# Performance work log

Measured on AMD Instinct MI355X. Metric: run time of the kernel, lower is better.

The kernel has to match this reference:

```python
import jax, jax.numpy as jnp
import numpy as np

B, L, EMBED = 8, 4096, 1024
HEADS, WIN, SHIFT = 16, 128, 64
HD = EMBED // HEADS
MLP_HIDDEN = 4 * EMBED
SCALE = HD ** -0.5
NW = L // WIN


def _layer_norm(x, w, b, eps=1e-5):
    m = x.mean(-1, keepdims=True)
    v = x.var(-1, keepdims=True)
    return (x - m) * jax.lax.rsqrt(v + eps) * w + b


def _compute_mask():
    # replicate SwinBlock1D._compute_mask: region ids over full L, then windowed
    sizes = [L - WIN, WIN - SHIFT, SHIFT]
    region = np.zeros(L, np.int32)
    pos = 0
    for i, s in enumerate(sizes):
        region[pos:pos + s] = i
        pos += s
    region = region.reshape(NW, WIN)
    diff = region[:, None, :] - region[:, :, None]  # (nW, W, W)
    return jnp.asarray(np.where(diff != 0, -100.0, 0.0).astype(np.float32))


_MASK = _compute_mask()
_REL_IDX = jnp.arange(WIN)[None, :] - jnp.arange(WIN)[:, None] + WIN - 1  # (W, W)


def setup_inputs() -> dict:
    key = jax.random.key(0)
    ks = jax.random.split(key, 8)
    s = 0.02

    def w(k, shape):
        return jax.random.normal(k, shape, jnp.float32) * s

    return {
        "x": jax.random.normal(ks[0], (B, L, EMBED), jnp.float32),
        "qkv_w": w(ks[1], (3 * EMBED, EMBED)),
        "qkv_b": jnp.zeros((3 * EMBED,), jnp.float32),
        "proj_w": w(ks[2], (EMBED, EMBED)),
        "proj_b": jnp.zeros((EMBED,), jnp.float32),
        "rpb": w(ks[3], (2 * WIN - 1, HEADS)),
        "norm1_w": jnp.ones((EMBED,), jnp.float32),
        "norm1_b": jnp.zeros((EMBED,), jnp.float32),
        "norm2_w": jnp.ones((EMBED,), jnp.float32),
        "norm2_b": jnp.zeros((EMBED,), jnp.float32),
        "mlp_w1": w(ks[4], (MLP_HIDDEN, EMBED)),
        "mlp_b1": jnp.zeros((MLP_HIDDEN,), jnp.float32),
        "mlp_w2": w(ks[5], (EMBED, MLP_HIDDEN)),
        "mlp_b2": jnp.zeros((EMBED,), jnp.float32),
    }


def reference(x, qkv_w, qkv_b, proj_w, proj_b, rpb,
              norm1_w, norm1_b, norm2_w, norm2_b,
              mlp_w1, mlp_b1, mlp_w2, mlp_b2):
    BW = B * NW
    shortcut = x
    h = _layer_norm(x, norm1_w, norm1_b)
    # shifted-window attention (shift_size > 0)
    h = jnp.roll(h, -SHIFT, axis=1)
    win = h.reshape(BW, WIN, EMBED)
    qkv = (win @ qkv_w.T + qkv_b).reshape(BW, WIN, 3, HEADS, HD)
    qkv = qkv.transpose(2, 0, 3, 1, 4)  # (3, BW, H, W, hd)
    q, k, v = qkv[0], qkv[1], qkv[2]
    attn = jnp.einsum('bhqd,bhkd->bhqk', q, k) * SCALE
    bias = rpb[_REL_IDX]  # (W, W, H)
    attn = attn + bias.transpose(2, 0, 1)[None]
    attn = attn.reshape(B, NW, HEADS, WIN, WIN) + _MASK[None, :, None]
    attn = jax.nn.softmax(attn.reshape(BW, HEADS, WIN, WIN), axis=-1)
    # dropout layers are identity in eval mode
    out = jnp.einsum('bhqk,bhkd->bhqd', attn, v)
    out = out.transpose(0, 2, 1, 3).reshape(BW, WIN, EMBED)
    out = out @ proj_w.T + proj_b
    out = out.reshape(B, L, EMBED)
    out = jnp.roll(out, SHIFT, axis=1)
    x = shortcut + out
    # MLP block
    h2 = _layer_norm(x, norm2_w, norm2_b)
    h2 = jax.nn.gelu(h2 @ mlp_w1.T + mlp_b1, approximate=False) @ mlp_w2.T + mlp_b2
    return x + h2
```

## Files before the change

### kernel.cpp

```cpp
#include <hip/hip_runtime.h>
#include <cstdint>
#include <cstddef>

#define SEQ_L   4096
#define EMBED   1024
#define HEADS   16
#define WINSZ   128
#define SHIFTSZ 64
#define HD      64
#define NWIN    32
#define MTOT    32768
#define ATT_SCALE 0.125f

typedef __bf16 bf16x8 __attribute__((ext_vector_type(8)));
typedef float  f32x4  __attribute__((ext_vector_type(4)));

typedef __attribute__((address_space(3))) void       lds_void;
typedef const __attribute__((address_space(1))) void gbl_void;

#define GLDS16(g, s) __builtin_amdgcn_global_load_lds((gbl_void*)(g), (lds_void*)(s), 16, 0, 0)

__device__ __forceinline__ unsigned short f2bf(float f) {
    unsigned int u = __float_as_uint(f);
    u += 0x7fffu + ((u >> 16) & 1u);
    return (unsigned short)(u >> 16);
}

__launch_bounds__(256)
__global__ void wconv(const float* __restrict__ in, unsigned short* __restrict__ out, int n)
{
    const int i = (blockIdx.x * 256 + threadIdx.x) * 4;
    if (i < n) {
        const float4 v = *(const float4*)(in + i);
        ushort4 o;
        o.x = f2bf(v.x); o.y = f2bf(v.y); o.z = f2bf(v.z); o.w = f2bf(v.w);
        *(ushort4*)(out + i) = o;
    }
}

__launch_bounds__(256)
__global__ void ln_kernel(const float* __restrict__ x, const float* __restrict__ gw,
                          const float* __restrict__ gb, unsigned short* __restrict__ out,
                          int shift)
{
    const int row  = blockIdx.x * 4 + (threadIdx.x >> 6);
    const int lane = threadIdx.x & 63;
    const int b    = row >> 12;
    const int lw   = row & 4095;
    const int src  = (b << 12) | ((lw + shift) & 4095);
    const float* xr = x + (size_t)src * EMBED;

    float4 v[4];
    float s = 0.f, q = 0.f;
#pragma unroll
    for (int j = 0; j < 4; ++j) {
        v[j] = ((const float4*)xr)[lane + j * 64];
        s += v[j].x + v[j].y + v[j].z + v[j].w;
        q += v[j].x * v[j].x + v[j].y * v[j].y + v[j].z * v[j].z + v[j].w * v[j].w;
    }
#pragma unroll
    for (int off = 32; off > 0; off >>= 1) {
        s += __shfl_xor(s, off);
        q += __shfl_xor(q, off);
    }
    const float mean = s * (1.0f / 1024.0f);
    const float rstd = rsqrtf(q * (1.0f / 1024.0f) - mean * mean + 1e-5f);

    unsigned short* orow = out + (size_t)row * EMBED;
#pragma unroll
    for (int j = 0; j < 4; ++j) {
        const float4 w4 = ((const float4*)gw)[lane + j * 64];
        const float4 b4 = ((const float4*)gb)[lane + j * 64];
        ushort4 o;
        o.x = f2bf((v[j].x - mean) * rstd * w4.x + b4.x);
        o.y = f2bf((v[j].y - mean) * rstd * w4.y + b4.y);
        o.z = f2bf((v[j].z - mean) * rstd * w4.z + b4.z);
        o.w = f2bf((v[j].w - mean) * rstd * w4.w + b4.w);
        ((ushort4*)orow)[lane + j * 64] = o;
    }
}


__device__ __forceinline__ void stage_half(const unsigned short* __restrict__ g, int ldk,
                                           char* ldsbase, int tid)
{
    const int r  = tid >> 3;
    const int cg = ((tid & 7) ^ (r & 7)) << 3;
    GLDS16(g + (size_t)r        * ldk + cg, ldsbase + tid * 16);
    GLDS16(g + (size_t)(r + 64) * ldk + cg, ldsbase + 8192 + tid * 16);
}

__device__ __forceinline__ bf16x8 lds_frag(const char* half, int row, int koff)
{
    const int off = koff ^ ((row & 7) << 4);
    return *(const bf16x8*)(half + row * 128 + off);
}

template<int EPI>
__launch_bounds__(512, 2)
__global__ void gemm256(const unsigned short* __restrict__ A, const unsigned short* __restrict__ W,
                        const float* __restrict__ bias, void* __restrict__ outv,
                        const float* __restrict__ resid, int M, int N, int K)
{
    __shared__ __align__(16) char lds[131072];
    const int tid = threadIdx.x;
    const int l   = tid & 63, w = tid >> 6;
    const int wm  = w >> 2, wn = w & 3;
    const int lr  = l & 15, hi = l >> 4;
    const int k0off = hi << 4;
    const int br0   = (wn & 1) << 6;

    int id = blockIdx.x;
    const int nwg = gridDim.x;
    id = (id & 7) * (nwg >> 3) + (id >> 3);
    const int Ntl = N >> 8;
    const int m0  = (id / Ntl) << 8;
    const int n0  = (id % Ntl) << 8;
    const int NT  = K >> 6;

#define HTB(b, ab, h) (lds + ((((b) << 1 | (ab)) << 1 | (h)) << 14))

    stage_half(A + (size_t)m0         * K,      K, HTB(0,0,0), tid);
    stage_half(A + (size_t)(m0 + 128) * K,      K, HTB(0,0,1), tid);
    stage_half(W + (size_t)n0         * K,      K, HTB(0,1,0), tid);
    stage_half(W + (size_t)(n0 + 128) * K,      K, HTB(0,1,1), tid);
    stage_half(W + (size_t)n0         * K + 64, K, HTB(1,1,0), tid);
    stage_half(W + (size_t)(n0 + 128) * K + 64, K, HTB(1,1,1), tid);
    asm volatile("s_waitcnt vmcnt(4)" ::: "memory");
    __builtin_amdgcn_s_barrier();

    f32x4 acc[8][4];
#pragma unroll
    for (int f = 0; f < 8; ++f)
#pragma unroll
        for (int n = 0; n < 4; ++n)
            acc[f][n] = (f32x4){0.f, 0.f, 0.f, 0.f};

    bf16x8 bf[4][2], af0[2][2], af1[2][2];

#define LOAD_A_BANK(bank, AHP, F0)                                          \
    af##bank[0][0] = lds_frag(AHP, (F0) * 16 + lr,      k0off);             \
    af##bank[0][1] = lds_frag(AHP, (F0) * 16 + lr,      64 + k0off);        \
    af##bank[1][0] = lds_frag(AHP, (F0) * 16 + 16 + lr, k0off);             \
    af##bank[1][1] = lds_frag(AHP, (F0) * 16 + 16 + lr, 64 + k0off);

#define MFMA_BANK(bank, F0)                                                 \
    __builtin_amdgcn_s_setprio(1);                                          \
    _Pragma("unroll")                                                       \
    for (int n = 0; n < 4; ++n) {                                           \
        acc[F0][n]     = __builtin_amdgcn_mfma_f32_16x16x32_bf16(af##bank[0][0], bf[n][0], acc[F0][n], 0, 0, 0);         \
        acc[F0][n]     = __builtin_amdgcn_mfma_f32_16x16x32_bf16(af##bank[0][1], bf[n][1], acc[F0][n], 0, 0, 0);         \
        acc[(F0) + 1][n] = __builtin_amdgcn_mfma_f32_16x16x32_bf16(af##bank[1][0], bf[n][0], acc[(F0) + 1][n], 0, 0, 0); \
        acc[(F0) + 1][n] = __builtin_amdgcn_mfma_f32_16x16x32_bf16(af##bank[1][1], bf[n][1], acc[(F0) + 1][n], 0, 0, 0); \
    }                                                                       \
    __builtin_amdgcn_s_setprio(0);

    {
        const char* Bh0 = HTB(0, 1, wn >> 1);
#pragma unroll
        for (int n = 0; n < 4; ++n) {
            bf[n][0] = lds_frag(Bh0, br0 + n * 16 + lr, k0off);
            bf[n][1] = lds_frag(Bh0, br0 + n * 16 + lr, 64 + k0off);
        }
        const char* Ah0 = HTB(0, 0, wm);
        LOAD_A_BANK(0, Ah0, 0)
    }

#define TILE(BUF)                                                              \
    {                                                                          \
        const char* Ah = HTB(BUF, 0, wm);                                      \
        const unsigned short* An = A + (size_t)m0 * K + (size_t)(t + 1) * 64;  \
        const unsigned short* Wn = W + (size_t)n0 * K + (size_t)(t + 2) * 64;  \
                                                        \
        LOAD_A_BANK(1, Ah, 2)                                                  \
        if (t + 1 < NT) stage_half(An, K, HTB(BUF ^ 1, 0, 0), tid);            \
        asm volatile("s_waitcnt lgkmcnt(4)" ::: "memory");                     \
        MFMA_BANK(0, 0)                                                        \
        __builtin_amdgcn_s_barrier();                                          \
                                                        \
        LOAD_A_BANK(0, Ah, 4)                                                  \
        if (t + 1 < NT) stage_half(An + (size_t)128 * K, K, HTB(BUF ^ 1, 0, 1), tid); \
        asm volatile("s_waitcnt lgkmcnt(4)" ::: "memory");                     \
        MFMA_BANK(1, 2)                                                        \
        __builtin_amdgcn_s_barrier();                                          \
                                                        \
        LOAD_A_BANK(1, Ah, 6)                                                  \
        if (t + 2 < NT) stage_half(Wn, K, HTB(BUF, 1, 0), tid);                \
        asm volatile("s_waitcnt lgkmcnt(4)" ::: "memory");                     \
        MFMA_BANK(0, 4)                                                        \
        __builtin_amdgcn_s_barrier();                                          \
                                                        \
        if (t + 2 < NT) { asm volatile("s_waitcnt vmcnt(2)" ::: "memory"); }   \
        else            { asm volatile("s_waitcnt vmcnt(0)" ::: "memory"); }   \
        if (t + 1 < NT) { const char* AhN = HTB(BUF ^ 1, 0, wm); LOAD_A_BANK(0, AhN, 0) } \
        if (t + 2 < NT) stage_half(Wn + (size_t)128 * K, K, HTB(BUF, 1, 1), tid); \
        if (t + 1 < NT) { asm volatile("s_waitcnt lgkmcnt(4)" ::: "memory"); } \
        else            { asm volatile("s_waitcnt lgkmcnt(0)" ::: "memory"); } \
        MFMA_BANK(1, 6)                                                        \
        if (t + 1 < NT) {                                                      \
            const char* BhN = HTB(BUF ^ 1, 1, wn >> 1);                        \
            _Pragma("unroll")                                                  \
            for (int n = 0; n < 4; ++n) {                                      \
                bf[n][0] = lds_frag(BhN, br0 + n * 16 + lr, k0off);            \
                bf[n][1] = lds_frag(BhN, br0 + n * 16 + lr, 64 + k0off);       \
            }                                                                  \
        }                                                                      \
        __builtin_amdgcn_s_barrier();                                          \
    }

    int t;
    for (int u = 0; u < (NT >> 1); ++u) {
        t = 2 * u;     TILE(0)
        t = 2 * u + 1; TILE(1)
    }
#undef TILE
#undef LOAD_A_BANK
#undef MFMA_BANK
#undef HTB

    const int cb = n0 + wn * 64;
    float bv[4];
#pragma unroll
    for (int n = 0; n < 4; ++n) bv[n] = bias[cb + n * 16 + lr];

#pragma unroll
    for (int f = 0; f < 8; ++f) {
        const int mbase = m0 + wm * 128 + f * 16 + hi * 4;
#pragma unroll
        for (int n = 0; n < 4; ++n) {
            const int col = cb + n * 16 + lr;
#pragma unroll
            for (int r = 0; r < 4; ++r) {
                const int m = mbase + r;
                float v = acc[f][n][r] + bv[n];
                if constexpr (EPI == 0) {
                    ((unsigned short*)outv)[(size_t)m * N + col] = f2bf(v);
                } else if constexpr (EPI == 1) {
                    const int bb = m >> 12;
                    const int lw = m & 4095;
                    const int ll = (lw + SHIFTSZ) & 4095;
                    const size_t di = ((size_t)(bb << 12) + ll) * (size_t)N + col;
                    ((float*)outv)[di] = resid[di] + v;
                } else if constexpr (EPI == 2) {
                    const float g = 0.5f * v * (1.0f + erff(v * 0.70710678118654752f));
                    ((unsigned short*)outv)[(size_t)m * N + col] = f2bf(g);
                } else {
                    float* o = (float*)outv;
                    const size_t di = (size_t)m * N + col;
                    o[di] = o[di] + v;
                }
            }
        }
    }
}

__device__ __forceinline__ bf16x8 vt_frag(const char* vt, int d, int kbyte)
{
    const int key = ((d >> 3) & 7) << 4;
    return *(const bf16x8*)(vt + d * 272 + (kbyte ^ key));
}

__launch_bounds__(256, 2)
__global__ void attn_kernel(const unsigned short* __restrict__ qkv, const float* __restrict__ rpb,
                            unsigned short* __restrict__ outp)
{
    __shared__ __align__(16) char          Ks[128 * 128];
    __shared__ __align__(16) unsigned short P[WINSZ][136];
    __shared__ __align__(16) unsigned short VTl[64 * 136];

    const int t   = threadIdx.x;
    const int l   = t & 63;
    const int w   = t >> 6;
    const int lr  = l & 15;
    const int lq  = l >> 4;
    const int lk  = lq * 8;
    const int blk = blockIdx.x;
    const int win = blk >> 4;
    const int h   = blk & 15;
    const bool masked = ((win & (NWIN - 1)) == NWIN - 1);

    const unsigned short* qb = qkv + (size_t)(win * WINSZ) * (3 * EMBED) + h * HD;
    const unsigned short* kb = qb + EMBED;
    const unsigned short* vb = qb + 2 * EMBED;

    {
        const int c = t & 7;
#pragma unroll
        for (int p = 0; p < 4; ++p) {
            const int r  = (t >> 3) + p * 32;
            const int cg = (c ^ (r & 7)) << 3;
            GLDS16(kb + (size_t)r * (3 * EMBED) + cg, Ks + p * 4096 + t * 16);
        }
    }
    {
        const int c = t & 7;
#pragma unroll
        for (int p = 0; p < 4; ++p) {
            const int k = (t >> 3) + p * 32;
            const uint4 v = *(const uint4*)(vb + (size_t)k * (3 * EMBED) + c * 8);
            const unsigned int vals[4] = {v.x, v.y, v.z, v.w};
            char* base = (char*)VTl;
#pragma unroll
            for (int e2 = 0; e2 < 4; ++e2) {
                const int d0 = c * 8 + e2 * 2;
                const int key = c << 4;
                *(unsigned short*)(base + d0 * 272 + ((2 * k) ^ key))       = (unsigned short)(vals[e2] & 0xffff);
                *(unsigned short*)(base + (d0 + 1) * 272 + ((2 * k) ^ key)) = (unsigned short)(vals[e2] >> 16);
            }
        }
    }
    asm volatile("s_waitcnt vmcnt(0)" ::: "memory");
    __syncthreads();

    const int mrow = w * 32;
    f32x4 sacc[2][8];
#pragma unroll
    for (int a = 0; a < 2; ++a)
#pragma unroll
        for (int b = 0; b < 8; ++b)
            sacc[a][b] = (f32x4){0.f, 0.f, 0.f, 0.f};

#pragma unroll
    for (int ks = 0; ks < 2; ++ks) {
        const int kby = ks * 64 + lq * 16;
        bf16x8 aq[2], bk8[8];
#pragma unroll
        for (int mi = 0; mi < 2; ++mi)
            aq[mi] = *(const bf16x8*)(qb + (size_t)(mrow + mi * 16 + lr) * (3 * EMBED) + ks * 32 + lk);
#pragma unroll
        for (int ni = 0; ni < 8; ++ni)
            bk8[ni] = lds_frag(Ks, ni * 16 + lr, kby);
#pragma unroll
        for (int mi = 0; mi < 2; ++mi)
#pragma unroll
            for (int ni = 0; ni < 8; ++ni)
                sacc[mi][ni] = __builtin_amdgcn_mfma_f32_16x16x32_bf16(aq[mi], bk8[ni], sacc[mi][ni], 0, 0, 0);
    }

#pragma unroll
    for (int mi = 0; mi < 2; ++mi)
#pragma unroll
        for (int r = 0; r < 4; ++r) {
            const int i = mrow + mi * 16 + lq * 4 + r;
            float v[8];
            float mx = -1e30f;
#pragma unroll
            for (int ni = 0; ni < 8; ++ni) {
                const int j = ni * 16 + lr;
                float sv = sacc[mi][ni][r] * ATT_SCALE + rpb[(j - i + WINSZ - 1) * HEADS + h];
                if (masked && ((i >= SHIFTSZ) != (j >= SHIFTSZ))) sv -= 100.0f;
                v[ni] = sv;
                mx = fmaxf(mx, sv);
            }
#pragma unroll
            for (int s = 1; s < 16; s <<= 1) mx = fmaxf(mx, __shfl_xor(mx, s));
            float sm = 0.f;
#pragma unroll
            for (int ni = 0; ni < 8; ++ni) {
                const float p = __expf(v[ni] - mx);
                v[ni] = p;
                sm += p;
            }
#pragma unroll
            for (int s = 1; s < 16; s <<= 1) sm += __shfl_xor(sm, s);
            const float rs = 1.0f / sm;
#pragma unroll
            for (int ni = 0; ni < 8; ++ni)
                P[i][ni * 16 + lr] = f2bf(v[ni] * rs);
        }

    __syncthreads();

    f32x4 oacc[2][4];
#pragma unroll
    for (int a = 0; a < 2; ++a)
#pragma unroll
        for (int b = 0; b < 4; ++b)
            oacc[a][b] = (f32x4){0.f, 0.f, 0.f, 0.f};

#pragma unroll
    for (int ks = 0; ks < 4; ++ks) {
        const int k0 = ks * 32;
        bf16x8 ap[2], av[4];
#pragma unroll
        for (int mi = 0; mi < 2; ++mi)
            ap[mi] = *(const bf16x8*)(&P[mrow + mi * 16 + lr][k0 + lk]);
#pragma unroll
        for (int ni = 0; ni < 4; ++ni)
            av[ni] = vt_frag((const char*)VTl, ni * 16 + lr, k0 * 2 + lq * 16);
#pragma unroll
        for (int mi = 0; mi < 2; ++mi)
#pragma unroll
            for (int ni = 0; ni < 4; ++ni)
                oacc[mi][ni] = __builtin_amdgcn_mfma_f32_16x16x32_bf16(ap[mi], av[ni], oacc[mi][ni], 0, 0, 0);
    }

    unsigned short* ob = outp + (size_t)(win * WINSZ) * EMBED + h * HD;
#pragma unroll
    for (int mi = 0; mi < 2; ++mi)
#pragma unroll
        for (int ni = 0; ni < 4; ++ni)
#pragma unroll
            for (int r = 0; r < 4; ++r) {
                const int i = mrow + mi * 16 + lq * 4 + r;
                const int d = ni * 16 + lr;
                ob[(size_t)i * EMBED + d] = f2bf(oacc[mi][ni][r]);
            }
}

extern "C" void kernel_launch(void* const* d_in, const int* in_sizes, int n_in,
                              void* d_out, int out_size, void* d_ws, size_t ws_size,
                              hipStream_t stream)
{
    const float* x      = (const float*)d_in[0];
    const float* qkv_w  = (const float*)d_in[1];
    const float* qkv_b  = (const float*)d_in[2];
    const float* proj_w = (const float*)d_in[3];
    const float* proj_b = (const float*)d_in[4];
    const float* rpb    = (const float*)d_in[5];
    const float* n1w    = (const float*)d_in[6];
    const float* n1b    = (const float*)d_in[7];
    const float* n2w    = (const float*)d_in[8];
    const float* n2b    = (const float*)d_in[9];
    const float* w1     = (const float*)d_in[10];
    const float* b1     = (const float*)d_in[11];
    const float* w2     = (const float*)d_in[12];
    const float* b2     = (const float*)d_in[13];
    float* out = (float*)d_out;

    unsigned short* wqkv  = (unsigned short*)d_ws;
    unsigned short* wproj = wqkv  + (size_t)3072 * 1024;
    unsigned short* wm1   = wproj + (size_t)1024 * 1024;
    unsigned short* wm2   = wm1   + (size_t)4096 * 1024;
    unsigned short* bufA  = wm2   + (size_t)4096 * 1024;
    unsigned short* bufB  = bufA  + (size_t)MTOT * EMBED;

    wconv<<<3072, 256, 0, stream>>>(qkv_w, wqkv, 3 * EMBED * EMBED);
    wconv<<<1024, 256, 0, stream>>>(proj_w, wproj, EMBED * EMBED);
    wconv<<<4096, 256, 0, stream>>>(w1, wm1, 4 * EMBED * EMBED);
    wconv<<<4096, 256, 0, stream>>>(w2, wm2, 4 * EMBED * EMBED);

    ln_kernel<<<8192, 256, 0, stream>>>(x, n1w, n1b, bufA, SHIFTSZ);

    gemm256<0><<<dim3(1536), 512, 0, stream>>>(bufA, wqkv, qkv_b, bufB, nullptr, MTOT, 3 * EMBED, EMBED);

    attn_kernel<<<4096, 256, 0, stream>>>(bufB, rpb, bufA);

    gemm256<1><<<dim3(512), 512, 0, stream>>>(bufA, wproj, proj_b, out, x, MTOT, EMBED, EMBED);

    ln_kernel<<<8192, 256, 0, stream>>>(out, n2w, n2b, bufA, 0);

    for (int c = 0; c < 2; ++c) {
        const size_t r0 = (size_t)c * 16384;
        gemm256<2><<<dim3(1024), 512, 0, stream>>>(bufA + r0 * EMBED, wm1, b1, bufB, nullptr,
                                                   16384, 4 * EMBED, EMBED);
        gemm256<3><<<dim3(256), 512, 0, stream>>>(bufB, wm2, b2, out + r0 * EMBED, nullptr,
                                                  16384, EMBED, 4 * EMBED);
    }
}
```

Baseline: 1.230 ms.

## Make GEMM persistent over 256 blocks with cross-tile prefetch and compile-time shapes

Converts the GEMM kernel into a persistent kernel launched with 256 workgroups, each processing TPB consecutive output tiles. The software pipeline now prefetches the next tile's A and W k-slices across tile boundaries, so loads continue while the previous tile's epilogue runs. K, N and the tile count become template parameters, which removes runtime division and lets the compiler specialise loops. The risk is fixed tile assignment: tail imbalance and L2 locality now depend on the hard-coded pid swizzle (blockIdx & 7)*32, which assumes exactly 256 blocks.

```diff
diff --git a/kernel.cpp b/kernel.cpp
--- a/kernel.cpp
+++ b/kernel.cpp
@@ -96,12 +96,17 @@
     return *(const bf16x8*)(half + row * 128 + off);
 }
 
-template<int EPI>
+template<int EPI, int K, int Ntl, int TPB>
 __launch_bounds__(512, 2)
 __global__ void gemm256(const unsigned short* __restrict__ A, const unsigned short* __restrict__ W,
                         const float* __restrict__ bias, void* __restrict__ outv,
-                        const float* __restrict__ resid, int M, int N, int K)
-{
+                        const float* __restrict__ resid)
+{
+    constexpr int N   = Ntl << 8;
+    constexpr int NT  = K >> 6;
+    constexpr int LNT = (NT == 16) ? 4 : 6;
+    constexpr int TT  = TPB * NT;
+
     __shared__ __align__(16) char lds[131072];
     const int tid = threadIdx.x;
     const int l   = tid & 63, w = tid >> 6;
@@ -110,22 +115,21 @@
     const int k0off = hi << 4;
     const int br0   = (wn & 1) << 6;
 
-    int id = blockIdx.x;
-    const int nwg = gridDim.x;
-    id = (id & 7) * (nwg >> 3) + (id >> 3);
-    const int Ntl = N >> 8;
-    const int m0  = (id / Ntl) << 8;
-    const int n0  = (id % Ntl) << 8;
-    const int NT  = K >> 6;
+    const int pid = (blockIdx.x & 7) * 32 + (blockIdx.x >> 3);
 
 #define HTB(b, ab, h) (lds + ((((b) << 1 | (ab)) << 1 | (h)) << 14))
 
-    stage_half(A + (size_t)m0         * K,      K, HTB(0,0,0), tid);
-    stage_half(A + (size_t)(m0 + 128) * K,      K, HTB(0,0,1), tid);
-    stage_half(W + (size_t)n0         * K,      K, HTB(0,1,0), tid);
-    stage_half(W + (size_t)(n0 + 128) * K,      K, HTB(0,1,1), tid);
-    stage_half(W + (size_t)n0         * K + 64, K, HTB(1,1,0), tid);
-    stage_half(W + (size_t)(n0 + 128) * K + 64, K, HTB(1,1,1), tid);
+    {
+        const int gid0 = pid * TPB;
+        const int m00  = (gid0 / Ntl) << 8;
+        const int n00  = (gid0 % Ntl) << 8;
+        stage_half(A + (size_t)m00         * K,      K, HTB(0,0,0), tid);
+        stage_half(A + (size_t)(m00 + 128) * K,      K, HTB(0,0,1), tid);
+        stage_half(W + (size_t)n00         * K,      K, HTB(0,1,0), tid);
+        stage_half(W + (size_t)(n00 + 128) * K,      K, HTB(0,1,1), tid);
+        stage_half(W + (size_t)n00         * K + 64, K, HTB(1,1,0), tid);
+        stage_half(W + (size_t)(n00 + 128) * K + 64, K, HTB(1,1,1), tid);
+    }
     asm volatile("s_waitcnt vmcnt(4)" ::: "memory");
     __builtin_amdgcn_s_barrier();
 
@@ -148,8 +152,8 @@
     __builtin_amdgcn_s_setprio(1);                                          \
     _Pragma("unroll")                                                       \
     for (int n = 0; n < 4; ++n) {                                           \
-        acc[F0][n]     = __builtin_amdgcn_mfma_f32_16x16x32_bf16(af##bank[0][0], bf[n][0], acc[F0][n], 0, 0, 0);         \
-        acc[F0][n]     = __builtin_amdgcn_mfma_f32_16x16x32_bf16(af##bank[0][1], bf[n][1], acc[F0][n], 0, 0, 0);         \
+        acc[F0][n]       = __builtin_amdgcn_mfma_f32_16x16x32_bf16(af##bank[0][0], bf[n][0], acc[F0][n], 0, 0, 0);       \
+        acc[F0][n]       = __builtin_amdgcn_mfma_f32_16x16x32_bf16(af##bank[0][1], bf[n][1], acc[F0][n], 0, 0, 0);       \
         acc[(F0) + 1][n] = __builtin_amdgcn_mfma_f32_16x16x32_bf16(af##bank[1][0], bf[n][0], acc[(F0) + 1][n], 0, 0, 0); \
         acc[(F0) + 1][n] = __builtin_amdgcn_mfma_f32_16x16x32_bf16(af##bank[1][1], bf[n][1], acc[(F0) + 1][n], 0, 0, 0); \
     }                                                                       \
@@ -168,36 +172,46 @@
 
 #define TILE(BUF)                                                              \
     {                                                                          \
+        const int F  = q * NT + t;                                             \
+        const int f1 = F + 1, f2 = F + 2;                                      \
         const char* Ah = HTB(BUF, 0, wm);                                      \
-        const unsigned short* An = A + (size_t)m0 * K + (size_t)(t + 1) * 64;  \
-        const unsigned short* Wn = W + (size_t)n0 * K + (size_t)(t + 2) * 64;  \
+        const unsigned short* An = nullptr;                                    \
+        const unsigned short* Wn = nullptr;                                    \
+        if (f1 < TT) {                                                         \
+            const int g1 = pid * TPB + (f1 >> LNT);                            \
+            An = A + (size_t)((g1 / Ntl) << 8) * K + (size_t)(f1 & (NT - 1)) * 64; \
+        }                                                                      \
+        if (f2 < TT) {                                                         \
+            const int g2 = pid * TPB + (f2 >> LNT);                            \
+            Wn = W + (size_t)((g2 % Ntl) << 8) * K + (size_t)(f2 & (NT - 1)) * 64; \
+        }                                                                      \
                                                         \
         LOAD_A_BANK(1, Ah, 2)                                                  \
-        if (t + 1 < NT) stage_half(An, K, HTB(BUF ^ 1, 0, 0), tid);            \
+        if (f1 < TT) stage_half(An, K, HTB(BUF ^ 1, 0, 0), tid);               \
         asm volatile("s_waitcnt lgkmcnt(4)" ::: "memory");                     \
         MFMA_BANK(0, 0)                                                        \
         __builtin_amdgcn_s_barrier();                                          \
                                                         \
         LOAD_A_BANK(0, Ah, 4)                                                  \
-        if (t + 1 < NT) stage_half(An + (size_t)128 * K, K, HTB(BUF ^ 1, 0, 1), tid); \
+        if (f1 < TT) stage_half(An + (size_t)128 * K, K, HTB(BUF ^ 1, 0, 1), tid); \
         asm volatile("s_waitcnt lgkmcnt(4)" ::: "memory");                     \
         MFMA_BANK(1, 2)                                                        \
         __builtin_amdgcn_s_barrier();                                          \
                                                         \
         LOAD_A_BANK(1, Ah, 6)                                                  \
-        if (t + 2 < NT) stage_half(Wn, K, HTB(BUF, 1, 0), tid);                \
+        if (f2 < TT) stage_half(Wn, K, HTB(BUF, 1, 0), tid);                   \
         asm volatile("s_waitcnt lgkmcnt(4)" ::: "memory");                     \
         MFMA_BANK(0, 4)                                                        \
         __builtin_amdgcn_s_barrier();                                          \
                                                         \
-        if (t + 2 < NT) { asm volatile("s_waitcnt vmcnt(2)" ::: "memory"); }   \
-        else            { asm volatile("s_waitcnt vmcnt(0)" ::: "memory"); }   \
-        if (t + 1 < NT) { const char* AhN = HTB(BUF ^ 1, 0, wm); LOAD_A_BANK(0, AhN, 0) } \
-        if (t + 2 < NT) stage_half(Wn + (size_t)128 * K, K, HTB(BUF, 1, 1), tid); \
-        if (t + 1 < NT) { asm volatile("s_waitcnt lgkmcnt(4)" ::: "memory"); } \
-        else            { asm volatile("s_waitcnt lgkmcnt(0)" ::: "memory"); } \
+        if (f2 < TT)      { asm volatile("s_waitcnt vmcnt(2)" ::: "memory"); } \
+        else              { asm volatile("s_waitcnt vmcnt(0)" ::: "memory"); } \
+        if (f1 < TT) { const char* AhN = HTB(BUF ^ 1, 0, wm); LOAD_A_BANK(0, AhN, 0) } \
+        if (f2 < TT) stage_half(Wn + (size_t)128 * K, K, HTB(BUF, 1, 1), tid); \
+        if (f1 < TT) { asm volatile("s_waitcnt lgkmcnt(4)" ::: "memory"); }    \
+        else         { asm volatile("s_waitcnt lgkmcnt(0)" ::: "memory"); }    \
         MFMA_BANK(1, 6)                                                        \
-        if (t + 1 < NT) {                                                      \
+        if (f1 < TT) {                                                         \
             const char* BhN = HTB(BUF ^ 1, 1, wn >> 1);                        \
             _Pragma("unroll")                                                  \
             for (int n = 0; n < 4; ++n) {                                      \
@@ -208,50 +222,64 @@
         __builtin_amdgcn_s_barrier();                                          \
     }
 
-    int t;
-    for (int u = 0; u < (NT >> 1); ++u) {
-        t = 2 * u;     TILE(0)
-        t = 2 * u + 1; TILE(1)
+#pragma unroll 1
+    for (int q = 0; q < TPB; ++q) {
+        int t;
+#pragma unroll 1
+        for (int u = 0; u < (NT >> 1); ++u) {
+            t = 2 * u;     TILE(0)
+            t = 2 * u + 1; TILE(1)
+        }
+
+        {
+            const int gid = pid * TPB + q;
+            const int m0e = (gid / Ntl) << 8;
+            const int n0e = (gid % Ntl) << 8;
+            const int cb  = n0e + wn * 64;
+            float bv[4];
+#pragma unroll
+            for (int n = 0; n < 4; ++n) bv[n] = bias[cb + n * 16 + lr];
+
+#pragma unroll
+            for (int f = 0; f < 8; ++f) {
+                const int mbase = m0e + wm * 128 + f * 16 + hi * 4;
+#pragma unroll
+                for (int n = 0; n < 4; ++n) {
+                    const int col = cb + n * 16 + lr;
+#pragma unroll
+                    for (int r = 0; r < 4; ++r) {
+                        const int m = mbase + r;
+                        float v = acc[f][n][r] + bv[n];
+                        if constexpr (EPI == 0) {
+                            ((unsigned short*)outv)[(size_t)m * N + col] = f2bf(v);
+                        } else if constexpr (EPI == 1) {
+                            const int bb = m >> 12;
+                            const int lw = m & 4095;
+                            const int ll = (lw + SHIFTSZ) & 4095;
+                            const size_t di = ((size_t)(bb << 12) + ll) * (size_t)N + col;
+                            ((float*)outv)[di] = resid[di] + v;
+                        } else if constexpr (EPI == 2) {
+                            const float g = 0.5f * v * (1.0f + erff(v * 0.70710678118654752f));
+                            ((unsigned short*)outv)[(size_t)m * N + col] = f2bf(g);
+                        } else {
+                            float* o = (float*)outv;
+                            const size_t di = (size_t)m * N + col;
+                            o[di] = o[di] + v;
+                        }
+                    }
+                }
+            }
+#pragma unroll
+            for (int f = 0; f < 8; ++f)
+#pragma unroll
+                for (int n = 0; n < 4; ++n)
+                    acc[f][n] = (f32x4){0.f, 0.f, 0.f, 0.f};
+        }
     }
 #undef TILE
 #undef LOAD_A_BANK
 #undef MFMA_BANK
 #undef HTB
-
-    const int cb = n0 + wn * 64;
-    float bv[4];
-#pragma unroll
-    for (int n = 0; n < 4; ++n) bv[n] = bias[cb + n * 16 + lr];
-
-#pragma unroll
-    for (int f = 0; f < 8; ++f) {
-        const int mbase = m0 + wm * 128 + f * 16 + hi * 4;
-#pragma unroll
-        for (int n = 0; n < 4; ++n) {
-            const int col = cb + n * 16 + lr;
-#pragma unroll
-            for (int r = 0; r < 4; ++r) {
-                const int m = mbase + r;
-                float v = acc[f][n][r] + bv[n];
-                if constexpr (EPI == 0) {
-                    ((unsigned short*)outv)[(size_t)m * N + col] = f2bf(v);
-                } else if constexpr (EPI == 1) {
-                    const int bb = m >> 12;
-                    const int lw = m & 4095;
-                    const int ll = (lw + SHIFTSZ) & 4095;
-                    const size_t di = ((size_t)(bb << 12) + ll) * (size_t)N + col;
-                    ((float*)outv)[di] = resid[di] + v;
-                } else if constexpr (EPI == 2) {
-                    const float g = 0.5f * v * (1.0f + erff(v * 0.70710678118654752f));
-                    ((unsigned short*)outv)[(size_t)m * N + col] = f2bf(g);
-                } else {
-                    float* o = (float*)outv;
-                    const size_t di = (size_t)m * N + col;
-                    o[di] = o[di] + v;
-                }
-            }
-        }
-    }
 }
 
 __device__ __forceinline__ bf16x8 vt_frag(const char* vt, int d, int kbyte)
@@ -442,19 +470,17 @@
 
     ln_kernel<<<8192, 256, 0, stream>>>(x, n1w, n1b, bufA, SHIFTSZ);
 
-    gemm256<0><<<dim3(1536), 512, 0, stream>>>(bufA, wqkv, qkv_b, bufB, nullptr, MTOT, 3 * EMBED, EMBED);
+    gemm256<0, 1024, 12, 6><<<256, 512, 0, stream>>>(bufA, wqkv, qkv_b, bufB, nullptr);
 
     attn_kernel<<<4096, 256, 0, stream>>>(bufB, rpb, bufA);
 
-    gemm256<1><<<dim3(512), 512, 0, stream>>>(bufA, wproj, proj_b, out, x, MTOT, EMBED, EMBED);
+    gemm256<1, 1024, 4, 2><<<256, 512, 0, stream>>>(bufA, wproj, proj_b, out, x);
 
     ln_kernel<<<8192, 256, 0, stream>>>(out, n2w, n2b, bufA, 0);
 
     for (int c = 0; c < 2; ++c) {
         const size_t r0 = (size_t)c * 16384;
-        gemm256<2><<<dim3(1024), 512, 0, stream>>>(bufA + r0 * EMBED, wm1, b1, bufB, nullptr,
-                                                   16384, 4 * EMBED, EMBED);
-        gemm256<3><<<dim3(256), 512, 0, stream>>>(bufB, wm2, b2, out + r0 * EMBED, nullptr,
-                                                  16384, EMBED, 4 * EMBED);
-    }
-}
+        gemm256<2, 1024, 16, 4><<<256, 512, 0, stream>>>(bufA + r0 * EMBED, wm1, b1, bufB, nullptr);
+        gemm256<3, 4096, 4, 1><<<256, 512, 0, stream>>>(bufB, wm2, b2, out + r0 * EMBED, nullptr);
+    }
+}
```

Result: slower. 1.277 ms (+3.8%).
